# Performance work log

Hardware: AMD Instinct MI355X
Metric: run time of the kernel (lower is better)

## Reference

```python
import jax, jax.numpy as jnp
import numpy as np

NHEADS = 8
HEAD_DIM = 64  # odim // nheads = 512 // 8


def setup_inputs() -> dict:
    key = jax.random.key(0)
    ks = jax.random.split(key, 5)
    B, S, D = 2, 4096, 512
    scale = 1.0 / np.sqrt(D)
    return {
        "m_feats": jax.random.normal(ks[0], (B, S, D), dtype=jnp.float32),
        "Wc": jax.random.normal(ks[1], (2 * D, D), dtype=jnp.float32) * scale,
        "bc": jax.random.normal(ks[2], (2 * D,), dtype=jnp.float32) * 0.01,
        "Wv": jax.random.normal(ks[3], (D, D), dtype=jnp.float32) * scale,
        "bv": jax.random.normal(ks[4], (D,), dtype=jnp.float32) * 0.01,
    }


def reference(m_feats, Wc, bc, Wv, bv):
    # eval mode: dropout(p=0.5) is identity
    B, S, D = m_feats.shape
    H, Dh = NHEADS, HEAD_DIM
    m_k = m_feats @ Wv.T + bv                    # [B,S,D]
    m_trans = m_feats @ Wc.T + bc                # [B,S,2D]
    m_q, m_v = m_trans[..., :D], m_trans[..., D:]
    # torch.split into contiguous per-head chunks == reshape to [B,S,H,Dh]
    k = m_k.reshape(B, S, H, Dh)
    q = m_q.reshape(B, S, H, Dh)
    v = m_v.reshape(B, S, H, Dh)
    # scores[b,h,i,j] = k_i . q_j / sqrt(Dh); softmax over j (the q axis)
    scores = jnp.einsum("bihd,bjhd->bhij", k, q) / np.sqrt(Dh).astype(np.float32)
    w = jax.nn.softmax(scores, axis=-1)          # [B,H,S,S]
    r = jnp.einsum("bhij,bjhd->bihd", w, v).reshape(B, S, D)
    return m_feats + r
```

## Files before the change

### kernel.cpp

```cpp
#include <hip/hip_runtime.h>

#define MTOT 8192

typedef __attribute__((ext_vector_type(8))) short bf16x8;
typedef __attribute__((ext_vector_type(4))) float f32x4;

#if __has_builtin(__builtin_amdgcn_exp2f)
#define EXP2F __builtin_amdgcn_exp2f
#else
#define EXP2F exp2f
#endif

#define SC 0.18033688011112042f
#define LDP 72
#define CTS 136
#define CTQ 72

static __device__ __forceinline__ unsigned short tb(float f) {
  union { float f; unsigned int i; } x;
  x.f = f;
  return (unsigned short)(x.i >> 16);
}
static __device__ __forceinline__ unsigned int pkt(float a, float b) {
  union { float f; unsigned int i; } xa, xb;
  xa.f = a; xb.f = b;
  return (xa.i >> 16) | (xb.i & 0xFFFF0000u);
}
static __device__ __forceinline__ bf16x8 ld8f32_bf16(const float* __restrict__ p) {
  f32x4 lo = *(const f32x4*)p;
  f32x4 hi = *(const f32x4*)(p + 4);
  union { unsigned int u[4]; bf16x8 v; } r;
  r.u[0] = pkt(lo[0], lo[1]);
  r.u[1] = pkt(lo[2], lo[3]);
  r.u[2] = pkt(hi[0], hi[1]);
  r.u[3] = pkt(hi[2], hi[3]);
  return r.v;
}

static __device__ __forceinline__ void stage16(const unsigned short* g,
                                               unsigned short* l, int lane) {
#if __has_builtin(__builtin_amdgcn_global_load_lds)
  __builtin_amdgcn_global_load_lds(
      (const __attribute__((address_space(1))) void*)g,
      (__attribute__((address_space(3))) void*)l, 16, 0, 0);
#else
  *(uint4*)(l + lane * 8) = *(const uint4*)g;
#endif
}

__global__ __launch_bounds__(256) void convert_bf16(
    const float* __restrict__ mf,
    const float* __restrict__ Wc,
    const float* __restrict__ Wv,
    unsigned short* __restrict__ dst)
{
  const size_t NA = (size_t)MTOT * 512;
  const size_t NW = (size_t)1536 * 512;
  const size_t total = (NA + NW) / 8;
  for (size_t u = (size_t)blockIdx.x * blockDim.x + threadIdx.x; u < total;
       u += (size_t)gridDim.x * blockDim.x) {
    const size_t el = u * 8;
    const float* src;
    if (el < NA) {
      src = mf + el;
    } else {
      const size_t e2 = el - NA;
      src = (e2 < (size_t)1024 * 512) ? (Wc + e2) : (Wv + (e2 - (size_t)1024 * 512));
    }
    f32x4 lo = *(const f32x4*)src;
    f32x4 hi = *(const f32x4*)(src + 4);
    uint4 pk;
    pk.x = pkt(lo[0], lo[1]); pk.y = pkt(lo[2], lo[3]);
    pk.z = pkt(hi[0], hi[1]); pk.w = pkt(hi[2], hi[3]);
    *(uint4*)(dst + el) = pk;
  }
}

__global__ __launch_bounds__(256) void gemm_fast(
    const unsigned short* __restrict__ Abf,
    const unsigned short* __restrict__ Wbf,
    const float* __restrict__ bc,
    const float* __restrict__ bv,
    unsigned short* __restrict__ ws)
{
  const int cpx = (int)gridDim.x >> 3;
  const int bid = ((int)blockIdx.x & 7) * cpx + ((int)blockIdx.x >> 3);
  const int tn = bid % 24, tm = bid / 24;
  const int w = threadIdx.x >> 6, lane = threadIdx.x & 63;
  const int n = lane & 15, q = lane >> 4;

  __shared__ alignas(16) unsigned short smem[128 * 64 + 64 * 64];
  unsigned short* As = smem;
  unsigned short* Bs = smem + 128 * 64;

  f32x4 acc[4][2] = {};
  const int rowA0 = tm * 128, colB0 = tn * 64;
  const int lrow = lane >> 3;
  const int sw = ((lane & 7) ^ lrow) * 8;
  const unsigned short* gA = Abf + (size_t)(rowA0 + w * 32 + lrow) * 512 + sw;
  const unsigned short* gB = Wbf + (size_t)(colB0 + w * 16 + lrow) * 512 + sw;

  for (int kc = 0; kc < 512; kc += 64) {
#pragma unroll
    for (int rr = 0; rr < 4; ++rr)
      stage16(gA + (size_t)rr * 8 * 512 + kc, As + (w * 32 + rr * 8) * 64, lane);
#pragma unroll
    for (int rr = 0; rr < 2; ++rr)
      stage16(gB + (size_t)rr * 8 * 512 + kc, Bs + (w * 16 + rr * 8) * 64, lane);
    __syncthreads();
#pragma unroll
    for (int ks = 0; ks < 2; ++ks) {
      const int ch = ((ks * 4 + q) ^ (n & 7)) * 8;
      bf16x8 a[4], b[2];
#pragma unroll
      for (int si = 0; si < 4; ++si)
        a[si] = *(const bf16x8*)(&As[((w >> 1) * 64 + si * 16 + n) * 64 + ch]);
#pragma unroll
      for (int sj = 0; sj < 2; ++sj)
        b[sj] = *(const bf16x8*)(&Bs[((w & 1) * 32 + sj * 16 + n) * 64 + ch]);
#pragma unroll
      for (int si = 0; si < 4; ++si)
#pragma unroll
        for (int sj = 0; sj < 2; ++sj)
          acc[si][sj] = __builtin_amdgcn_mfma_f32_16x16x32_bf16(a[si], b[sj], acc[si][sj], 0, 0, 0);
    }
    __syncthreads();
  }

  unsigned short* Ct = smem;
  const bool isV = (tn >= 8 && tn < 16);
  const int rl0 = (w >> 1) * 64, cl0 = (w & 1) * 32;

  if (!isV) {
    const bool isK = (tn >= 16);
#pragma unroll
    for (int sj = 0; sj < 2; ++sj) {
      const int c = colB0 + cl0 + sj * 16 + n;
      const float bias = isK ? bv[c - 1024] : bc[c];
#pragma unroll
      for (int si = 0; si < 4; ++si)
#pragma unroll
        for (int r = 0; r < 4; ++r) {
          float v = acc[si][sj][r] + bias;
          if (isK) v *= SC;
          Ct[(rl0 + si * 16 + q * 4 + r) * CTQ + cl0 + sj * 16 + n] = tb(v);
        }
    }
  } else {
#pragma unroll
    for (int sj = 0; sj < 2; ++sj) {
      const float bias = bc[colB0 + cl0 + sj * 16 + n];
#pragma unroll
      for (int si = 0; si < 4; ++si) {
        uint2 pk;
        pk.x = pkt(acc[si][sj][0] + bias, acc[si][sj][1] + bias);
        pk.y = pkt(acc[si][sj][2] + bias, acc[si][sj][3] + bias);
        *(uint2*)(&Ct[(cl0 + sj * 16 + n) * CTS + rl0 + si * 16 + q * 4]) = pk;
      }
    }
  }
  __syncthreads();

  if (!isV) {
    const int rk = threadIdx.x & 7, rr2 = threadIdx.x >> 3;
#pragma unroll
    for (int rp = 0; rp < 4; ++rp) {
      const int row = rp * 32 + rr2;
      const int col = rk * 8;
      bf16x8 v = *(const bf16x8*)(&Ct[row * CTQ + col]);
      const int srow = rowA0 + row;
      const int bb = srow >> 12, ss = srow & 4095;
      const int cg = colB0 + col;
      const int cl = (cg >= 1024) ? (cg - 1024) : cg;
      const int hh = cl >> 6, dh0 = cl & 63;
      unsigned short* base = (cg >= 1024) ? (ws + (size_t)2 * MTOT * 512) : ws;
      *(bf16x8*)(base + ((size_t)((bb * 8 + hh) * 4096 + ss)) * 64 + dh0) = v;
    }
  } else {
    const int rk = threadIdx.x & 15, rr2 = threadIdx.x >> 4;
#pragma unroll
    for (int rp = 0; rp < 4; ++rp) {
      const int row = rp * 16 + rr2;
      const int col = rk * 8;
      bf16x8 v = *(const bf16x8*)(&Ct[row * CTS + col]);
      const int cv = (tn - 8) * 64 + row;
      const int hh = cv >> 6, dh0 = cv & 63;
      const int sg = rowA0 + col;
      const int bb = sg >> 12, ss = sg & 4095;
      *(bf16x8*)(ws + (size_t)MTOT * 512 +
                 ((size_t)((bb * 8 + hh) * 64 + dh0)) * 4096 + ss) = v;
    }
  }
}

__global__ __launch_bounds__(256) void gemm_qvk(
    const float* __restrict__ mf,
    const float* __restrict__ Wc,
    const float* __restrict__ bc,
    const float* __restrict__ Wv,
    const float* __restrict__ bv,
    unsigned short* __restrict__ ws,
    int nct)
{
  const int cpx = (int)gridDim.x >> 3;
  const int bid = ((int)blockIdx.x & 7) * cpx + ((int)blockIdx.x >> 3);
  const int tn = bid % nct, tm = bid / nct;
  const int w = threadIdx.x >> 6, lane = threadIdx.x & 63;
  const int n = lane & 15, q = lane >> 4;

  __shared__ alignas(16) unsigned short smem[2 * 128 * LDP];
  unsigned short* As = smem;
  unsigned short* Bs = smem + 128 * LDP;

  f32x4 acc[4][4] = {};
  const int rowA0 = tm * 128, colB0 = tn * 128;
  const int sr = threadIdx.x >> 4;
  const int sc = (threadIdx.x & 15) * 4;

  for (int kc = 0; kc < 512; kc += 64) {
    __syncthreads();
#pragma unroll
    for (int rr = 0; rr < 8; ++rr) {
      const int row = rr * 16 + sr;
      f32x4 av = *(const f32x4*)(mf + (size_t)(rowA0 + row) * 512 + kc + sc);
      uint2 ap; ap.x = pkt(av[0], av[1]); ap.y = pkt(av[2], av[3]);
      *(uint2*)(&As[row * LDP + sc]) = ap;
      const int c = colB0 + row;
      const float* bsrc = (c < 1024) ? (Wc + (size_t)c * 512)
                                     : (Wv + (size_t)(c - 1024) * 512);
      f32x4 bvx = *(const f32x4*)(bsrc + kc + sc);
      uint2 bp; bp.x = pkt(bvx[0], bvx[1]); bp.y = pkt(bvx[2], bvx[3]);
      *(uint2*)(&Bs[row * LDP + sc]) = bp;
    }
    __syncthreads();
#pragma unroll
    for (int ks = 0; ks < 2; ++ks) {
      bf16x8 a[4], b[4];
#pragma unroll
      for (int si = 0; si < 4; ++si)
        a[si] = *(const bf16x8*)(&As[((w >> 1) * 64 + si * 16 + n) * LDP + ks * 32 + q * 8]);
#pragma unroll
      for (int sj = 0; sj < 4; ++sj)
        b[sj] = *(const bf16x8*)(&Bs[((w & 1) * 64 + sj * 16 + n) * LDP + ks * 32 + q * 8]);
#pragma unroll
      for (int si = 0; si < 4; ++si)
#pragma unroll
        for (int sj = 0; sj < 4; ++sj)
          acc[si][sj] = __builtin_amdgcn_mfma_f32_16x16x32_bf16(a[si], b[sj], acc[si][sj], 0, 0, 0);
    }
  }

  __syncthreads();
  unsigned short* Ct = smem;
  const bool isV = (tn >= 4 && tn < 8);
  const int rl0 = (w >> 1) * 64, cl0 = (w & 1) * 64;

  if (!isV) {
    const bool isK = (tn >= 8);
#pragma unroll
    for (int sj = 0; sj < 4; ++sj) {
      const int c = colB0 + cl0 + sj * 16 + n;
      const float bias = isK ? bv[c - 1024] : bc[c];
#pragma unroll
      for (int si = 0; si < 4; ++si)
#pragma unroll
        for (int r = 0; r < 4; ++r) {
          float v = acc[si][sj][r] + bias;
          if (isK) v *= SC;
          Ct[(rl0 + si * 16 + q * 4 + r) * CTS + cl0 + sj * 16 + n] = tb(v);
        }
    }
  } else {
#pragma unroll
    for (int sj = 0; sj < 4; ++sj) {
      const float bias = bc[colB0 + cl0 + sj * 16 + n];
#pragma unroll
      for (int si = 0; si < 4; ++si) {
        uint2 pk;
        pk.x = pkt(acc[si][sj][0] + bias, acc[si][sj][1] + bias);
        pk.y = pkt(acc[si][sj][2] + bias, acc[si][sj][3] + bias);
        *(uint2*)(&Ct[(cl0 + sj * 16 + n) * CTS + rl0 + si * 16 + q * 4]) = pk;
      }
    }
  }
  __syncthreads();

  const int rk = threadIdx.x & 7, rr2 = threadIdx.x >> 3;
#pragma unroll
  for (int rp = 0; rp < 4; ++rp) {
    const int row = rp * 32 + rr2;
#pragma unroll
    for (int ch = 0; ch < 2; ++ch) {
      const int col = ch * 64 + rk * 8;
      bf16x8 v = *(const bf16x8*)(&Ct[row * CTS + col]);
      if (!isV) {
        const int srow = rowA0 + row;
        const int bb = srow >> 12, ss = srow & 4095;
        const int cg = colB0 + col;
        const int cl = (cg >= 1024) ? (cg - 1024) : cg;
        const int hh = cl >> 6, dh0 = cl & 63;
        unsigned short* base = (cg >= 1024) ? (ws + (size_t)2 * MTOT * 512) : ws;
        *(bf16x8*)(base + ((size_t)((bb * 8 + hh) * 4096 + ss)) * 64 + dh0) = v;
      } else {
        const int cv = (tn - 4) * 128 + row;
        const int hh = cv >> 6, dh0 = cv & 63;
        const int sg = rowA0 + col;
        const int bb = sg >> 12, ss = sg & 4095;
        *(bf16x8*)(ws + (size_t)MTOT * 512 +
                   ((size_t)((bb * 8 + hh) * 64 + dh0)) * 4096 + ss) = v;
      }
    }
  }
}

template <bool KWS>
__global__ __launch_bounds__(128, 2) void attn_kernel(
    const unsigned short* __restrict__ qvws,
    const float* __restrict__ mf,
    const float* __restrict__ Wv,
    const float* __restrict__ bv,
    float* __restrict__ out)
{
  const int bid = blockIdx.x;
  const int bh = ((bid & 7) << 1) | ((bid >> 3) & 1);
  const int ib = bid >> 4;
  const int b_ = bh >> 3, h = bh & 7;
  const int w = threadIdx.x >> 6, lane = threadIdx.x & 63;
  const int n = lane & 15, q = lane >> 4;
  const int i0 = ib * 64;

  __shared__ alignas(16) unsigned short PK[2][64 * LDP];
  __shared__ float lbuf[2][64];

  const unsigned short* Qb = qvws + (size_t)(bh * 4096) * 64;
  const unsigned short* Vb = qvws + (size_t)MTOT * 512 + (size_t)(bh * 64) * 4096;

  bf16x8 aK[4][2];
  if (KWS) {
    const unsigned short* Kb = qvws + (size_t)2 * MTOT * 512 + (size_t)(bh * 4096) * 64;
#pragma unroll
    for (int sub = 0; sub < 4; ++sub)
#pragma unroll
      for (int s = 0; s < 2; ++s)
        aK[sub][s] = *(const bf16x8*)(Kb + (size_t)(i0 + sub * 16 + n) * 64 + s * 32 + q * 8);
  } else {
    f32x4 ka[2][4] = {};
    for (int kk = 0; kk < 512; kk += 32) {
      bf16x8 a0 = ld8f32_bf16(mf + (size_t)(b_ * 4096 + i0 + (2 * w + 0) * 16 + n) * 512 + kk + q * 8);
      bf16x8 a1 = ld8f32_bf16(mf + (size_t)(b_ * 4096 + i0 + (2 * w + 1) * 16 + n) * 512 + kk + q * 8);
#pragma unroll
      for (int t = 0; t < 4; ++t) {
        bf16x8 bw = ld8f32_bf16(Wv + (size_t)(h * 64 + t * 16 + n) * 512 + kk + q * 8);
        ka[0][t] = __builtin_amdgcn_mfma_f32_16x16x32_bf16(a0, bw, ka[0][t], 0, 0, 0);
        ka[1][t] = __builtin_amdgcn_mfma_f32_16x16x32_bf16(a1, bw, ka[1][t], 0, 0, 0);
      }
    }
#pragma unroll
    for (int sl = 0; sl < 2; ++sl)
#pragma unroll
      for (int t = 0; t < 4; ++t) {
        const float bias = bv[h * 64 + t * 16 + n];
#pragma unroll
        for (int r = 0; r < 4; ++r)
          PK[0][((2 * w + sl) * 16 + q * 4 + r) * LDP + t * 16 + n] =
              tb((ka[sl][t][r] + bias) * SC);
      }
    __syncthreads();
#pragma unroll
    for (int sub = 0; sub < 4; ++sub)
#pragma unroll
      for (int s = 0; s < 2; ++s)
        aK[sub][s] = *(const bf16x8*)(&PK[0][(sub * 16 + n) * LDP + s * 32 + q * 8]);
    __syncthreads();
  }

  f32x4 o[4][4] = {};
  float lsc[4] = {0.0f, 0.0f, 0.0f, 0.0f};
  unsigned short* Pw = &PK[w][0];
  const int jbase = w * 2048;

  bf16x8 bq[4][2], bvv[4][2];
#pragma unroll
  for (int jt = 0; jt < 4; ++jt)
#pragma unroll
    for (int s = 0; s < 2; ++s)
      bq[jt][s] = *(const bf16x8*)(Qb + (size_t)(jbase + jt * 16 + n) * 64 + s * 32 + q * 8);
#pragma unroll
  for (int t = 0; t < 4; ++t)
#pragma unroll
    for (int s = 0; s < 2; ++s)
      bvv[t][s] = *(const bf16x8*)(Vb + (size_t)(t * 16 + n) * 4096 + jbase + s * 32 + q * 8);

  for (int it = 0; it < 32; ++it) {
    const int j1 = jbase + ((it + 1) & 31) * 64;

    f32x4 c[2][4];
#pragma unroll
    for (int jt = 0; jt < 4; ++jt) {
      f32x4 z = {};
      z = __builtin_amdgcn_mfma_f32_16x16x32_bf16(bq[jt][0], aK[0][0], z, 0, 0, 0);
      z = __builtin_amdgcn_mfma_f32_16x16x32_bf16(bq[jt][1], aK[0][1], z, 0, 0, 0);
      c[0][jt] = z;
    }

#pragma unroll
    for (int sub = 0; sub < 4; ++sub) {
      const int cur = sub & 1, nxt = cur ^ 1;
      if (sub < 3) {
#pragma unroll
        for (int jt = 0; jt < 4; ++jt) {
          f32x4 z = {};
          z = __builtin_amdgcn_mfma_f32_16x16x32_bf16(bq[jt][0], aK[sub + 1][0], z, 0, 0, 0);
          z = __builtin_amdgcn_mfma_f32_16x16x32_bf16(bq[jt][1], aK[sub + 1][1], z, 0, 0, 0);
          c[nxt][jt] = z;
        }
      }
      if (sub == 2) {
#pragma unroll
        for (int jt = 0; jt < 4; ++jt)
#pragma unroll
          for (int s = 0; s < 2; ++s)
            bq[jt][s] = *(const bf16x8*)(Qb + (size_t)(j1 + jt * 16 + n) * 64 + s * 32 + q * 8);
      }

#pragma unroll
      for (int jt = 0; jt < 4; ++jt) {
        float e0 = EXP2F(c[cur][jt][0]), e1 = EXP2F(c[cur][jt][1]);
        float e2 = EXP2F(c[cur][jt][2]), e3 = EXP2F(c[cur][jt][3]);
        lsc[sub] += (e0 + e1) + (e2 + e3);
        uint2 pk;
        pk.x = pkt(e0, e1);
        pk.y = pkt(e2, e3);
        *(uint2*)(Pw + (sub * 16 + n) * LDP + jt * 16 + q * 4) = pk;
      }
    }

    asm volatile("s_waitcnt lgkmcnt(0)" ::: "memory");

#pragma unroll
    for (int sub = 0; sub < 4; ++sub) {
#pragma unroll
      for (int s = 0; s < 2; ++s) {
        bf16x8 pa = *(const bf16x8*)(Pw + (sub * 16 + n) * LDP + s * 32 + q * 8);
#pragma unroll
        for (int t = 0; t < 4; ++t)
          o[sub][t] = __builtin_amdgcn_mfma_f32_16x16x32_bf16(pa, bvv[t][s], o[sub][t], 0, 0, 0);
      }
    }

#pragma unroll
    for (int t = 0; t < 4; ++t)
#pragma unroll
      for (int s = 0; s < 2; ++s)
        bvv[t][s] = *(const bf16x8*)(Vb + (size_t)(t * 16 + n) * 4096 + j1 + s * 32 + q * 8);
  }

  float lw[4];
#pragma unroll
  for (int sub = 0; sub < 4; ++sub) {
    float v = lsc[sub];
    v += __shfl_xor(v, 16, 64);
    v += __shfl_xor(v, 32, 64);
    lw[sub] = v;
  }

  __syncthreads();
  float* mO = (float*)&PK[0][0];
  const int ebase = (w == 0) ? 0 : 32;
  const int rbase = (w == 0) ? 32 : 0;
  const int esub0 = (w == 0) ? 2 : 0;
  const int ksub0 = (w == 0) ? 0 : 2;
#pragma unroll
  for (int sl = 0; sl < 2; ++sl) {
    const int sub = esub0 + sl;
#pragma unroll
    for (int t = 0; t < 4; ++t)
#pragma unroll
      for (int r = 0; r < 4; ++r)
        mO[(ebase + sl * 16 + q * 4 + r) * 68 + t * 16 + n] = o[sub][t][r];
  }
  if (lane < 16) {
#pragma unroll
    for (int sub = 0; sub < 4; ++sub)
      lbuf[w][sub * 16 + lane] = lw[sub];
  }
  __syncthreads();
#pragma unroll
  for (int sl = 0; sl < 2; ++sl) {
    const int sub = ksub0 + sl;
    float li[4];
#pragma unroll
    for (int r = 0; r < 4; ++r) {
      const int il = sub * 16 + q * 4 + r;
      li[r] = 1.0f / (lbuf[0][il] + lbuf[1][il]);
    }
#pragma unroll
    for (int t = 0; t < 4; ++t) {
#pragma unroll
      for (int r = 0; r < 4; ++r) {
        const int i = i0 + sub * 16 + q * 4 + r;
        const int dh = t * 16 + n;
        const size_t idx = (size_t)(b_ * 4096 + i) * 512 + h * 64 + dh;
        out[idx] = (o[sub][t][r] + mO[(rbase + sl * 16 + q * 4 + r) * 68 + t * 16 + n]) * li[r]
                   + mf[idx];
      }
    }
  }
}

extern "C" void kernel_launch(void* const* d_in, const int* in_sizes, int n_in,
                              void* d_out, int out_size, void* d_ws, size_t ws_size,
                              hipStream_t stream) {
  const float* mf = (const float*)d_in[0];
  const float* Wc = (const float*)d_in[1];
  const float* bc = (const float*)d_in[2];
  const float* Wv = (const float*)d_in[3];
  const float* bv = (const float*)d_in[4];
  float* out = (float*)d_out;
  unsigned short* ws = (unsigned short*)d_ws;

  const size_t elQ = (size_t)MTOT * 512;
  const bool kws = ws_size >= (size_t)3 * elQ * 2;

  if (kws) {
    unsigned short* Abf = (unsigned short*)out;
    unsigned short* Wbf = Abf + (size_t)MTOT * 512;
    convert_bf16<<<2048, 256, 0, stream>>>(mf, Wc, Wv, Abf);
    gemm_fast<<<1536, 256, 0, stream>>>(Abf, Wbf, bc, bv, ws);
    attn_kernel<true><<<1024, 128, 0, stream>>>(ws, mf, Wv, bv, out);
  } else {
    gemm_qvk<<<64 * 8, 256, 0, stream>>>(mf, Wc, bc, Wv, bv, ws, 8);
    attn_kernel<false><<<1024, 128, 0, stream>>>(ws, mf, Wv, bv, out);
  }
}
```

Baseline: 227.2 us.

## Switch attention inner loop to 32x32x16 MFMA with register-shuffled P operand

Rewrites the attention main loop to use 32x32x16 bf16 MFMA tiles instead of 16x16x32, processing 32 keys per iteration over 64 iterations. The exponentiated score tile is repacked into the A-operand layout for the PV MFMA with cross-lane shuffles instead of a round trip through LDS, which removes the per-iteration LDS write/read and waitcnt. The epilogue reduction buffer becomes a dedicated shared array. This trades LDS traffic for shuffle instructions and larger accumulator register footprint, which may affect occupancy under the 2-blocks launch bound.

```diff
diff --git a/kernel.cpp b/kernel.cpp
--- a/kernel.cpp
+++ b/kernel.cpp
@@ -4,6 +4,7 @@
 
 typedef __attribute__((ext_vector_type(8))) short bf16x8;
 typedef __attribute__((ext_vector_type(4))) float f32x4;
+typedef __attribute__((ext_vector_type(16))) float f32x16;
 
 #if __has_builtin(__builtin_amdgcn_exp2f)
 #define EXP2F __builtin_amdgcn_exp2f
@@ -323,27 +324,29 @@
 {
   const int bid = blockIdx.x;
   const int bh = ((bid & 7) << 1) | ((bid >> 3) & 1);
-  const int ib = bid >> 4;
+  const int ibt = bid >> 4;
   const int b_ = bh >> 3, h = bh & 7;
   const int w = threadIdx.x >> 6, lane = threadIdx.x & 63;
-  const int n = lane & 15, q = lane >> 4;
-  const int i0 = ib * 64;
-
-  __shared__ alignas(16) unsigned short PK[2][64 * LDP];
+  const int lo = lane & 31, hi = lane >> 5;
+  const int i0 = ibt * 64;
+
+  __shared__ alignas(16) unsigned short Kt[64 * LDP];
+  __shared__ alignas(16) float mO[64 * 68];
   __shared__ float lbuf[2][64];
 
   const unsigned short* Qb = qvws + (size_t)(bh * 4096) * 64;
   const unsigned short* Vb = qvws + (size_t)MTOT * 512 + (size_t)(bh * 64) * 4096;
 
-  bf16x8 aK[4][2];
+  bf16x8 aK[2][4];
   if (KWS) {
     const unsigned short* Kb = qvws + (size_t)2 * MTOT * 512 + (size_t)(bh * 4096) * 64;
 #pragma unroll
-    for (int sub = 0; sub < 4; ++sub)
-#pragma unroll
-      for (int s = 0; s < 2; ++s)
-        aK[sub][s] = *(const bf16x8*)(Kb + (size_t)(i0 + sub * 16 + n) * 64 + s * 32 + q * 8);
+    for (int ib = 0; ib < 2; ++ib)
+#pragma unroll
+      for (int cf = 0; cf < 4; ++cf)
+        aK[ib][cf] = *(const bf16x8*)(Kb + (size_t)(i0 + ib * 32 + lo) * 64 + cf * 16 + hi * 8);
   } else {
+    const int n = lane & 15, q = lane >> 4;
     f32x4 ka[2][4] = {};
     for (int kk = 0; kk < 512; kk += 32) {
       bf16x8 a0 = ld8f32_bf16(mf + (size_t)(b_ * 4096 + i0 + (2 * w + 0) * 16 + n) * 512 + kk + q * 8);
@@ -362,150 +365,130 @@
         const float bias = bv[h * 64 + t * 16 + n];
 #pragma unroll
         for (int r = 0; r < 4; ++r)
-          PK[0][((2 * w + sl) * 16 + q * 4 + r) * LDP + t * 16 + n] =
+          Kt[((2 * w + sl) * 16 + q * 4 + r) * LDP + t * 16 + n] =
               tb((ka[sl][t][r] + bias) * SC);
       }
     __syncthreads();
 #pragma unroll
-    for (int sub = 0; sub < 4; ++sub)
-#pragma unroll
-      for (int s = 0; s < 2; ++s)
-        aK[sub][s] = *(const bf16x8*)(&PK[0][(sub * 16 + n) * LDP + s * 32 + q * 8]);
-    __syncthreads();
-  }
-
-  f32x4 o[4][4] = {};
-  float lsc[4] = {0.0f, 0.0f, 0.0f, 0.0f};
-  unsigned short* Pw = &PK[w][0];
+    for (int ib = 0; ib < 2; ++ib)
+#pragma unroll
+      for (int cf = 0; cf < 4; ++cf)
+        aK[ib][cf] = *(const bf16x8*)(&Kt[(ib * 32 + lo) * LDP + cf * 16 + hi * 8]);
+  }
+
+  f32x16 o[2][2] = {};
+  float lsc[2] = {0.0f, 0.0f};
   const int jbase = w * 2048;
 
-  bf16x8 bq[4][2], bvv[4][2];
-#pragma unroll
-  for (int jt = 0; jt < 4; ++jt)
-#pragma unroll
-    for (int s = 0; s < 2; ++s)
-      bq[jt][s] = *(const bf16x8*)(Qb + (size_t)(jbase + jt * 16 + n) * 64 + s * 32 + q * 8);
-#pragma unroll
-  for (int t = 0; t < 4; ++t)
-#pragma unroll
-    for (int s = 0; s < 2; ++s)
-      bvv[t][s] = *(const bf16x8*)(Vb + (size_t)(t * 16 + n) * 4096 + jbase + s * 32 + q * 8);
-
-  for (int it = 0; it < 32; ++it) {
-    const int j1 = jbase + ((it + 1) & 31) * 64;
-
-    f32x4 c[2][4];
-#pragma unroll
-    for (int jt = 0; jt < 4; ++jt) {
-      f32x4 z = {};
-      z = __builtin_amdgcn_mfma_f32_16x16x32_bf16(bq[jt][0], aK[0][0], z, 0, 0, 0);
-      z = __builtin_amdgcn_mfma_f32_16x16x32_bf16(bq[jt][1], aK[0][1], z, 0, 0, 0);
-      c[0][jt] = z;
-    }
-
-#pragma unroll
-    for (int sub = 0; sub < 4; ++sub) {
-      const int cur = sub & 1, nxt = cur ^ 1;
-      if (sub < 3) {
-#pragma unroll
-        for (int jt = 0; jt < 4; ++jt) {
-          f32x4 z = {};
-          z = __builtin_amdgcn_mfma_f32_16x16x32_bf16(bq[jt][0], aK[sub + 1][0], z, 0, 0, 0);
-          z = __builtin_amdgcn_mfma_f32_16x16x32_bf16(bq[jt][1], aK[sub + 1][1], z, 0, 0, 0);
-          c[nxt][jt] = z;
-        }
-      }
-      if (sub == 2) {
-#pragma unroll
-        for (int jt = 0; jt < 4; ++jt)
-#pragma unroll
-          for (int s = 0; s < 2; ++s)
-            bq[jt][s] = *(const bf16x8*)(Qb + (size_t)(j1 + jt * 16 + n) * 64 + s * 32 + q * 8);
-      }
-
-#pragma unroll
-      for (int jt = 0; jt < 4; ++jt) {
-        float e0 = EXP2F(c[cur][jt][0]), e1 = EXP2F(c[cur][jt][1]);
-        float e2 = EXP2F(c[cur][jt][2]), e3 = EXP2F(c[cur][jt][3]);
-        lsc[sub] += (e0 + e1) + (e2 + e3);
-        uint2 pk;
-        pk.x = pkt(e0, e1);
-        pk.y = pkt(e2, e3);
-        *(uint2*)(Pw + (sub * 16 + n) * LDP + jt * 16 + q * 4) = pk;
-      }
-    }
-
-    asm volatile("s_waitcnt lgkmcnt(0)" ::: "memory");
-
-#pragma unroll
-    for (int sub = 0; sub < 4; ++sub) {
-#pragma unroll
-      for (int s = 0; s < 2; ++s) {
-        bf16x8 pa = *(const bf16x8*)(Pw + (sub * 16 + n) * LDP + s * 32 + q * 8);
-#pragma unroll
-        for (int t = 0; t < 4; ++t)
-          o[sub][t] = __builtin_amdgcn_mfma_f32_16x16x32_bf16(pa, bvv[t][s], o[sub][t], 0, 0, 0);
-      }
-    }
-
-#pragma unroll
-    for (int t = 0; t < 4; ++t)
-#pragma unroll
-      for (int s = 0; s < 2; ++s)
-        bvv[t][s] = *(const bf16x8*)(Vb + (size_t)(t * 16 + n) * 4096 + j1 + s * 32 + q * 8);
-  }
-
-  float lw[4];
-#pragma unroll
-  for (int sub = 0; sub < 4; ++sub) {
-    float v = lsc[sub];
-    v += __shfl_xor(v, 16, 64);
+  const unsigned short* qrow = Qb + (size_t)lo * 64 + hi * 8;
+  const unsigned short* vr0 = Vb + (size_t)(0 * 32 + lo) * 4096 + hi * 8;
+  const unsigned short* vr1 = Vb + (size_t)(1 * 32 + lo) * 4096 + hi * 8;
+
+  bf16x8 bq[4], bvv[2][2];
+#pragma unroll
+  for (int cf = 0; cf < 4; ++cf)
+    bq[cf] = *(const bf16x8*)(qrow + (size_t)jbase * 64 + cf * 16);
+#pragma unroll
+  for (int kf = 0; kf < 2; ++kf) {
+    bvv[0][kf] = *(const bf16x8*)(vr0 + jbase + kf * 16);
+    bvv[1][kf] = *(const bf16x8*)(vr1 + jbase + kf * 16);
+  }
+
+  for (int it = 0; it < 64; ++it) {
+    const int j1 = jbase + ((it + 1) & 63) * 32;
+
+    f32x16 c0 = {}, c1 = {};
+#pragma unroll
+    for (int cf = 0; cf < 4; ++cf)
+      c0 = __builtin_amdgcn_mfma_f32_32x32x16_bf16(bq[cf], aK[0][cf], c0, 0, 0, 0);
+#pragma unroll
+    for (int cf = 0; cf < 4; ++cf)
+      c1 = __builtin_amdgcn_mfma_f32_32x32x16_bf16(bq[cf], aK[1][cf], c1, 0, 0, 0);
+
+#pragma unroll
+    for (int cf = 0; cf < 4; ++cf)
+      bq[cf] = *(const bf16x8*)(qrow + (size_t)j1 * 64 + cf * 16);
+
+#pragma unroll
+    for (int ib = 0; ib < 2; ++ib) {
+      const f32x16 cc = ib ? c1 : c0;
+      float e[16];
+#pragma unroll
+      for (int r = 0; r < 16; ++r) e[r] = EXP2F(cc[r]);
+      float s = 0.0f;
+#pragma unroll
+      for (int r = 0; r < 16; ++r) s += e[r];
+      lsc[ib] += s;
+
+      unsigned int pk[8];
+#pragma unroll
+      for (int m = 0; m < 8; ++m) pk[m] = pkt(e[2 * m], e[2 * m + 1]);
+
+      unsigned int rcv[4];
+      rcv[0] = __shfl_xor(hi ? pk[0] : pk[2], 32, 64);
+      rcv[1] = __shfl_xor(hi ? pk[1] : pk[3], 32, 64);
+      rcv[2] = __shfl_xor(hi ? pk[4] : pk[6], 32, 64);
+      rcv[3] = __shfl_xor(hi ? pk[5] : pk[7], 32, 64);
+
+      union { uint4 u; bf16x8 v; } pa0, pa1;
+      pa0.u = hi ? make_uint4(rcv[0], rcv[1], pk[2], pk[3])
+                 : make_uint4(pk[0], pk[1], rcv[0], rcv[1]);
+      pa1.u = hi ? make_uint4(rcv[2], rcv[3], pk[6], pk[7])
+                 : make_uint4(pk[4], pk[5], rcv[2], rcv[3]);
+
+      o[ib][0] = __builtin_amdgcn_mfma_f32_32x32x16_bf16(pa0.v, bvv[0][0], o[ib][0], 0, 0, 0);
+      o[ib][1] = __builtin_amdgcn_mfma_f32_32x32x16_bf16(pa0.v, bvv[1][0], o[ib][1], 0, 0, 0);
+      o[ib][0] = __builtin_amdgcn_mfma_f32_32x32x16_bf16(pa1.v, bvv[0][1], o[ib][0], 0, 0, 0);
+      o[ib][1] = __builtin_amdgcn_mfma_f32_32x32x16_bf16(pa1.v, bvv[1][1], o[ib][1], 0, 0, 0);
+    }
+
+#pragma unroll
+    for (int kf = 0; kf < 2; ++kf) {
+      bvv[0][kf] = *(const bf16x8*)(vr0 + j1 + kf * 16);
+      bvv[1][kf] = *(const bf16x8*)(vr1 + j1 + kf * 16);
+    }
+  }
+
+  float lw[2];
+#pragma unroll
+  for (int ib = 0; ib < 2; ++ib) {
+    float v = lsc[ib];
     v += __shfl_xor(v, 32, 64);
-    lw[sub] = v;
+    lw[ib] = v;
   }
 
   __syncthreads();
-  float* mO = (float*)&PK[0][0];
-  const int ebase = (w == 0) ? 0 : 32;
-  const int rbase = (w == 0) ? 32 : 0;
-  const int esub0 = (w == 0) ? 2 : 0;
-  const int ksub0 = (w == 0) ? 0 : 2;
-#pragma unroll
-  for (int sl = 0; sl < 2; ++sl) {
-    const int sub = esub0 + sl;
-#pragma unroll
-    for (int t = 0; t < 4; ++t)
-#pragma unroll
-      for (int r = 0; r < 4; ++r)
-        mO[(ebase + sl * 16 + q * 4 + r) * 68 + t * 16 + n] = o[sub][t][r];
-  }
-  if (lane < 16) {
-#pragma unroll
-    for (int sub = 0; sub < 4; ++sub)
-      lbuf[w][sub * 16 + lane] = lw[sub];
+  const int esub = 1 - w, ksub = w;
+#pragma unroll
+  for (int df = 0; df < 2; ++df)
+#pragma unroll
+    for (int r = 0; r < 16; ++r) {
+      const int il = (r & 3) + 8 * (r >> 2) + 4 * hi;
+      mO[(esub * 32 + il) * 68 + df * 32 + lo] = o[esub][df][r];
+    }
+  if (lane < 32) {
+    lbuf[w][lane] = lw[0];
+    lbuf[w][32 + lane] = lw[1];
   }
   __syncthreads();
-#pragma unroll
-  for (int sl = 0; sl < 2; ++sl) {
-    const int sub = ksub0 + sl;
-    float li[4];
-#pragma unroll
-    for (int r = 0; r < 4; ++r) {
-      const int il = sub * 16 + q * 4 + r;
-      li[r] = 1.0f / (lbuf[0][il] + lbuf[1][il]);
-    }
-#pragma unroll
-    for (int t = 0; t < 4; ++t) {
-#pragma unroll
-      for (int r = 0; r < 4; ++r) {
-        const int i = i0 + sub * 16 + q * 4 + r;
-        const int dh = t * 16 + n;
-        const size_t idx = (size_t)(b_ * 4096 + i) * 512 + h * 64 + dh;
-        out[idx] = (o[sub][t][r] + mO[(rbase + sl * 16 + q * 4 + r) * 68 + t * 16 + n]) * li[r]
-                   + mf[idx];
-      }
-    }
-  }
+
+  float li[16];
+#pragma unroll
+  for (int r = 0; r < 16; ++r) {
+    const int il = ksub * 32 + (r & 3) + 8 * (r >> 2) + 4 * hi;
+    li[r] = 1.0f / (lbuf[0][il] + lbuf[1][il]);
+  }
+#pragma unroll
+  for (int df = 0; df < 2; ++df)
+#pragma unroll
+    for (int r = 0; r < 16; ++r) {
+      const int il = (r & 3) + 8 * (r >> 2) + 4 * hi;
+      const int i = i0 + ksub * 32 + il;
+      const int d = df * 32 + lo;
+      const size_t idx = (size_t)(b_ * 4096 + i) * 512 + h * 64 + d;
+      out[idx] = (o[ksub][df][r] + mO[(ksub * 32 + il) * 68 + df * 32 + lo]) * li[r]
+                 + mf[idx];
+    }
 }
 
 extern "C" void kernel_launch(void* const* d_in, const int* in_sizes, int n_in,
```

Result: slower. 239.5 us (+5.4%).
